# Optimization experiments

Hardware: AMD Instinct MI355X
Metric: run time of the kernel (lower is better)

Reference implementation:

```python
import jax, jax.numpy as jnp
import numpy as np

S = 4096            # num tokens (single causal sequence)
HID = 1024          # hidden_size
NH = 16             # num query heads
NKV = 4             # num kv heads
HD = 64             # head_dim
THETA = 10000.0
Q_SIZE = NH * HD
KV_SIZE = NKV * HD


def setup_inputs() -> dict:
    key = jax.random.key(0)
    k1, k2, k3 = jax.random.split(key, 3)
    return {
        "positions": jnp.arange(S, dtype=jnp.int32),
        "hidden_states": jax.random.normal(k1, (S, 2 * HID), dtype=jnp.float32),
        "w_qkv": jax.random.normal(k2, (Q_SIZE + 2 * KV_SIZE, 2 * HID), dtype=jnp.float32) * 0.02,
        "w_o": jax.random.normal(k3, (HID, Q_SIZE), dtype=jnp.float32) * 0.02,
    }


def _rope(x, positions):
    # x: [S, H, HD]; neox-style rotate-half RoPE
    half = HD // 2
    inv_freq = 1.0 / (THETA ** (jnp.arange(0, half, dtype=jnp.float32) / half))
    freqs = positions.astype(jnp.float32)[:, None] * inv_freq  # [S, half]
    cos = jnp.cos(freqs)[:, None, :]  # [S, 1, half]
    sin = jnp.sin(freqs)[:, None, :]
    x1, x2 = x[..., :half], x[..., half:]
    return jnp.concatenate([x1 * cos - x2 * sin, x2 * cos + x1 * sin], axis=-1)


def reference(positions, hidden_states, w_qkv, w_o):
    qkv = hidden_states @ w_qkv.T  # [S, Q_SIZE + 2*KV_SIZE]
    q = qkv[:, :Q_SIZE].reshape(S, NH, HD)
    k = qkv[:, Q_SIZE:Q_SIZE + KV_SIZE].reshape(S, NKV, HD)
    v = qkv[:, Q_SIZE + KV_SIZE:].reshape(S, NKV, HD)
    q = _rope(q, positions)
    k = _rope(k, positions)
    # GQA: group query heads over kv heads
    g = NH // NKV
    qg = q.reshape(S, NKV, g, HD)
    scale = HD ** -0.5
    scores = jnp.einsum("qhgd,thd->hgqt", qg, k) * scale  # [NKV, g, S, S]
    causal = positions[:, None] >= positions[None, :]      # [S, S]
    scores = jnp.where(causal[None, None], scores, jnp.finfo(scores.dtype).min)
    probs = jax.nn.softmax(scores, axis=-1)
    o = jnp.einsum("hgqt,thd->qhgd", probs, v).reshape(S, Q_SIZE)
    return o @ w_o.T  # [S, HID]
```

## Files before the change

### kernel.cpp

```cpp
#include <hip/hip_runtime.h>
#include <math.h>

#define S_LEN   4096
#define NHEADS  16
#define NKVH    4
#define HDIM    64
#define QKV_N   1536
#define HID2    2048
#define OUT_N   1024
#define QSCALE  0.18033688011112042f

typedef __attribute__((ext_vector_type(8))) __bf16 bf16x8;
typedef __attribute__((ext_vector_type(4))) __bf16 bf16x4;
typedef __attribute__((ext_vector_type(4))) float  f32x4;
typedef __attribute__((ext_vector_type(16))) float f32x16;
typedef __attribute__((ext_vector_type(4))) unsigned int u32x4;

#define GL_LDS16(gaddr, laddr)                                                  \
  __builtin_amdgcn_global_load_lds(                                             \
      (const __attribute__((address_space(1))) unsigned int*)(gaddr),           \
      (__attribute__((address_space(3))) unsigned int*)(laddr), 16, 0, 0)

__device__ __forceinline__ unsigned cvt_pk_bf16(float lo, float hi) {
  unsigned r;
  asm("v_cvt_pk_bf16_f32 %0, %1, %2" : "=v"(r) : "v"(lo), "v"(hi));
  return r;
}

__global__ __launch_bounds__(256) void cvt_all(const float* __restrict__ hid,
                                               const float* __restrict__ wq,
                                               const float* __restrict__ wo,
                                               __bf16* __restrict__ hid_bf,
                                               __bf16* __restrict__ wq_bf,
                                               __bf16* __restrict__ wo_bf) {
  const int n1 = S_LEN * HID2;
  const int n2 = QKV_N * HID2;
  int i = (blockIdx.x * blockDim.x + threadIdx.x) * 8;
  const float* src; __bf16* dst; int off;
  if (i < n1)           { src = hid; dst = hid_bf; off = i; }
  else if (i < n1 + n2) { src = wq;  dst = wq_bf;  off = i - n1; }
  else                  { src = wo;  dst = wo_bf;  off = i - n1 - n2; }
  float4 a = *(const float4*)(src + off);
  float4 b = *(const float4*)(src + off + 4);
  bf16x8 o = {(__bf16)a.x,(__bf16)a.y,(__bf16)a.z,(__bf16)a.w,
              (__bf16)b.x,(__bf16)b.y,(__bf16)b.z,(__bf16)b.w};
  *(bf16x8*)(dst + off) = o;
}

__global__ __launch_bounds__(256) void rope_table(const int* __restrict__ positions,
                                                  float* __restrict__ ct,
                                                  float* __restrict__ st) {
  int i = blockIdx.x * blockDim.x + threadIdx.x;
  int s = i >> 5, d = i & 31;
  double inv = pow(10000.0, -(double)d / 32.0);
  double fr = (double)positions[s] * inv;
  ct[i] = (float)cos(fr);
  st[i] = (float)sin(fr);
}

template<int BM, int EPI>
__global__ __launch_bounds__(256, (BM > 64 ? 2 : 3))
void gemm_db(const __bf16* __restrict__ A,
             const __bf16* __restrict__ B,
             void* __restrict__ Cp,
             const float* __restrict__ ct,
             const float* __restrict__ st,
             __bf16* __restrict__ qd,
             __bf16* __restrict__ kd,
             int M, int N, int K) {
  constexpr int TM  = BM / 32;
  constexpr int ASZ = BM * 32;
  constexpr int BSZ = 128 * 32;
  __shared__ __align__(16) __bf16 As[2 * 2 * ASZ];
  __shared__ __align__(16) __bf16 Bs[2 * 2 * BSZ];
  const int tid  = threadIdx.x;
  const int bm   = blockIdx.x, bn = blockIdx.y;
  const int wave = tid >> 6, lane = tid & 63;
  const int quad = lane >> 4, col = lane & 15;
  const int wm = (wave >> 1) * (BM / 2), wn = (wave & 1) * 64;

  const int lrow = lane >> 2, lcol = (lane & 3) * 8;
  const __bf16* Ag = A + (size_t)(bm * BM + wave * (BM / 4) + lrow) * K + lcol;
  const __bf16* Bg = B + (size_t)(bn * 128 + wave * 32 + lrow) * K + lcol;
  __bf16* AsW = As + wave * (BM / 4) * 32;
  __bf16* BsW = Bs + wave * 32 * 32;

  f32x4 acc[TM][4];
#pragma unroll
  for (int i = 0; i < TM; ++i)
#pragma unroll
    for (int j = 0; j < 4; ++j) acc[i][j] = (f32x4){0.f, 0.f, 0.f, 0.f};

  auto stage = [&](int buf, int kk) {
#pragma unroll
    for (int p = 0; p < 2; ++p) {
      const int koff = kk + p * 32;
      __bf16* ad = AsW + (buf * 2 + p) * ASZ;
      __bf16* bd = BsW + (buf * 2 + p) * BSZ;
#pragma unroll
      for (int u = 0; u < BM / 64; ++u)
        GL_LDS16(Ag + koff + (size_t)(u * 16) * K, ad + u * 16 * 32);
      GL_LDS16(Bg + koff,                  bd);
      GL_LDS16(Bg + koff + (size_t)16 * K, bd + 16 * 32);
    }
  };

  stage(0, 0);
  __syncthreads();

  int cur = 0;
  for (int kk = 0; kk < K; kk += 64) {
    if (kk + 64 < K) stage(cur ^ 1, kk + 64);

#pragma unroll
    for (int p = 0; p < 2; ++p) {
      const int pb = cur * 2 + p;
      bf16x8 a[TM], b[4];
#pragma unroll
      for (int tm = 0; tm < TM; ++tm)
        a[tm] = *(const bf16x8*)&As[pb * ASZ + (wm + tm * 16 + col) * 32 + quad * 8];
#pragma unroll
      for (int tn = 0; tn < 4; ++tn)
        b[tn] = *(const bf16x8*)&Bs[pb * BSZ + (wn + tn * 16 + col) * 32 + quad * 8];
#pragma unroll
      for (int tm = 0; tm < TM; ++tm)
#pragma unroll
        for (int tn = 0; tn < 4; ++tn)
          acc[tm][tn] = __builtin_amdgcn_mfma_f32_16x16x32_bf16(a[tm], b[tn], acc[tm][tn], 0, 0, 0);
    }

    __syncthreads();
    cur ^= 1;
  }

  if constexpr (EPI == 2) {
    if (bn < 10) {
      const float scl = (bn < 8) ? QSCALE : 1.0f;
      __bf16* dst    = (bn < 8) ? qd : kd;
      const int strd = (bn < 8) ? 1024 : 256;
      const int base = (bn < 8) ? 0 : 1024;
#pragma unroll
      for (int tm = 0; tm < TM; ++tm)
#pragma unroll
        for (int tn = 0; tn < 2; ++tn) {
          const int row0 = bm * BM + wm + tm * 16 + quad * 4;
          const int cg   = bn * 128 + wn + tn * 16 + col;
          const int dcol = cg - base;
          const int d    = tn * 16 + col;
#pragma unroll
          for (int r = 0; r < 4; ++r) {
            const int srow = row0 + r;
            float c  = ct[srow * 32 + d];
            float sn = st[srow * 32 + d];
            float x1 = acc[tm][tn][r], x2 = acc[tm][tn + 2][r];
            dst[(size_t)srow * strd + dcol]      = (__bf16)((x1 * c - x2 * sn) * scl);
            dst[(size_t)srow * strd + dcol + 32] = (__bf16)((x2 * c + x1 * sn) * scl);
          }
        }
    } else {
#pragma unroll
      for (int tm = 0; tm < TM; ++tm)
#pragma unroll
        for (int tn = 0; tn < 4; ++tn) {
          int row = bm * BM + wm + tm * 16 + quad * 4;
          int cg  = bn * 128 + wn + tn * 16 + col;
#pragma unroll
          for (int r = 0; r < 4; ++r)
            ((__bf16*)Cp)[(size_t)(row + r) * N + cg] = (__bf16)acc[tm][tn][r];
        }
    }
  } else {
#pragma unroll
    for (int tm = 0; tm < TM; ++tm)
#pragma unroll
      for (int tn = 0; tn < 4; ++tn) {
        int row = bm * BM + wm + tm * 16 + quad * 4;
        int cg  = bn * 128 + wn + tn * 16 + col;
#pragma unroll
        for (int r = 0; r < 4; ++r)
          ((float*)Cp)[(size_t)(row + r) * N + cg] = acc[tm][tn][r];
      }
  }
}

__global__ __launch_bounds__(256) void v_transpose(const __bf16* __restrict__ qkv,
                                                   __bf16* __restrict__ vT) {
  __shared__ __align__(16) __bf16 Ts[64][72];
  const int sb = blockIdx.x, kvh = blockIdx.y, t = threadIdx.x;
  const int r = t >> 2, c16 = (t & 3) * 16;
  const __bf16* src = qkv + (size_t)(sb * 64 + r) * QKV_N + 1280 + kvh * 64 + c16;
  bf16x8 v0 = *(const bf16x8*)src;
  bf16x8 v1 = *(const bf16x8*)(src + 8);
#pragma unroll
  for (int u = 0; u < 8; ++u) {
    Ts[c16 + u][r]     = v0[u];
    Ts[c16 + 8 + u][r] = v1[u];
  }
  __syncthreads();
  __bf16* dst = vT + ((size_t)kvh * 64 + r) * S_LEN + sb * 64 + c16;
  *(bf16x8*)dst       = *(const bf16x8*)&Ts[r][c16];
  *(bf16x8*)(dst + 8) = *(const bf16x8*)&Ts[r][c16 + 8];
}

__global__ __launch_bounds__(256, 4) void attn_split(const __bf16* __restrict__ qg,
                                                     const __bf16* __restrict__ kg,
                                                     const __bf16* __restrict__ vg,
                                                     __bf16* __restrict__ op0,
                                                     __bf16* __restrict__ op1,
                                                     float* __restrict__ lp) {
  __shared__ __align__(16) __bf16 lds[18432];
  __bf16* Ks = lds;
  __bf16* Vs = lds + 9216;

  const int tid = threadIdx.x;
  const int h = blockIdx.x;
  const int yy = blockIdx.y;
  const int qq = yy >> 1, split = yy & 1;
  const int qb = (qq < 16) ? qq : 47 - qq;
  const int kvh = h >> 2;
  const int wave = tid >> 6, lane = tid & 63;
  const int r31 = lane & 31, hi = lane >> 5;
  const int hi4 = hi * 4, hi8 = hi * 8;
  const int qbase = qb * 128 + wave * 32;
  const int kt0 = split * (qb + 1);
  const int ktEnd = kt0 + qb + 1;

  {
    const int r = tid >> 1, c = (tid & 1) * 32;
    const __bf16* src = qg + (size_t)(qb * 128 + r) * 1024 + h * 64 + c;
    __bf16* dq = lds + r * 72 + c;
    *(bf16x8*)(dq)      = *(const bf16x8*)(src);
    *(bf16x8*)(dq + 8)  = *(const bf16x8*)(src + 8);
    *(bf16x8*)(dq + 16) = *(const bf16x8*)(src + 16);
    *(bf16x8*)(dq + 24) = *(const bf16x8*)(src + 24);
  }

  const int sr = tid >> 2, sc = (tid & 3) * 16;
  const __bf16* kptr = kg + (size_t)sr * 256 + kvh * 64 + sc;
  const __bf16* vptr = vg + ((size_t)kvh * 64 + sr) * S_LEN + sc;
  bf16x8 kr0 = *(const bf16x8*)(kptr + (size_t)kt0 * 64 * 256);
  bf16x8 kr1 = *(const bf16x8*)(kptr + (size_t)kt0 * 64 * 256 + 8);
  bf16x8 vr0 = *(const bf16x8*)(vptr + (size_t)kt0 * 64);
  bf16x8 vr1 = *(const bf16x8*)(vptr + (size_t)kt0 * 64 + 8);

  __syncthreads();

  bf16x8 qf[4];
#pragma unroll
  for (int dc = 0; dc < 4; ++dc)
    qf[dc] = *(const bf16x8*)&lds[(wave * 32 + r31) * 72 + dc * 16 + hi8];

  __syncthreads();

  f32x16 fz;
#pragma unroll
  for (int g = 0; g < 16; ++g) fz[g] = 0.f;

  f32x16 o[2];
  o[0] = fz; o[1] = fz;
  float lacc = 0.f;

  for (int kt = kt0; kt < ktEnd; ++kt) {
    const int cur = (kt - kt0) & 1;
    {
      __bf16* kd = Ks + cur * 4608 + sr * 72 + sc;
      *(bf16x8*)kd       = kr0;
      *(bf16x8*)(kd + 8) = kr1;
      __bf16* vd = Vs + cur * 4608 + sr * 72 + sc;
      *(bf16x8*)vd       = vr0;
      *(bf16x8*)(vd + 8) = vr1;
    }
    if (kt + 1 < ktEnd) {
      const __bf16* kn = kptr + (size_t)(kt + 1) * 64 * 256;
      const __bf16* vn = vptr + (size_t)(kt + 1) * 64;
      kr0 = *(const bf16x8*)(kn);
      kr1 = *(const bf16x8*)(kn + 8);
      vr0 = *(const bf16x8*)(vn);
      vr1 = *(const bf16x8*)(vn + 8);
    }
    __syncthreads();

    if (kt * 64 > qbase + 31) continue;

    const bool full = (kt * 64 + 63 <= qbase);
    const int thr = qbase + r31 - kt * 64;

    bf16x8 pa[4];
#pragma unroll
    for (int kb = 0; kb < 2; ++kb) {
      bf16x8 kf0 = *(const bf16x8*)&Ks[cur * 4608 + (kb * 32 + r31) * 72 + hi8];
      f32x16 sf = __builtin_amdgcn_mfma_f32_32x32x16_bf16(kf0, qf[0], fz, 0, 0, 0);
#pragma unroll
      for (int dc = 1; dc < 4; ++dc) {
        bf16x8 kf = *(const bf16x8*)&Ks[cur * 4608 + (kb * 32 + r31) * 72 + dc * 16 + hi8];
        sf = __builtin_amdgcn_mfma_f32_32x32x16_bf16(kf, qf[dc], sf, 0, 0, 0);
      }
      float p[16];
#pragma unroll
      for (int g = 0; g < 16; ++g) {
        float e = __builtin_amdgcn_exp2f(sf[g]);
        if (!full) {
          const int krow = kb * 32 + (g & 3) + 8 * (g >> 2) + hi4;
          if (krow > thr) e = 0.f;
        }
        p[g] = e;
      }
#pragma unroll
      for (int m = 0; m < 4; ++m)
        lacc += (p[4 * m] + p[4 * m + 1]) + (p[4 * m + 2] + p[4 * m + 3]);
#pragma unroll
      for (int half = 0; half < 2; ++half) {
        unsigned a0 = cvt_pk_bf16(p[8 * half + 0], p[8 * half + 1]);
        unsigned a1 = cvt_pk_bf16(p[8 * half + 2], p[8 * half + 3]);
        unsigned b0 = cvt_pk_bf16(p[8 * half + 4], p[8 * half + 5]);
        unsigned b1 = cvt_pk_bf16(p[8 * half + 6], p[8 * half + 7]);
        asm("v_permlane32_swap_b32 %0, %1" : "+v"(a0), "+v"(b0));
        asm("v_permlane32_swap_b32 %0, %1" : "+v"(a1), "+v"(b1));
        u32x4 t = {a0, a1, b0, b1};
        pa[kb * 2 + half] = __builtin_bit_cast(bf16x8, t);
      }
    }

#pragma unroll
    for (int dt = 0; dt < 2; ++dt)
#pragma unroll
      for (int kc = 0; kc < 4; ++kc) {
        bf16x8 vf = *(const bf16x8*)&Vs[cur * 4608 + (dt * 32 + r31) * 72 + kc * 16 + hi8];
        o[dt] = __builtin_amdgcn_mfma_f32_32x32x16_bf16(pa[kc], vf, o[dt], 0, 0, 0);
      }
  }

  lacc += __shfl_xor(lacc, 32, 64);
  __syncthreads();
  float* lshw = (float*)lds + wave * 32;
  if (lane < 32) lshw[lane] = lacc;
  asm volatile("s_waitcnt lgkmcnt(0)" ::: "memory");

  __bf16* op = split ? op1 : op0;
#pragma unroll
  for (int g = 0; g < 16; ++g) {
    const int rl = (g & 3) + 8 * (g >> 2) + hi4;
    float l = lshw[rl];
    float linv = (l > 0.f) ? 1.f / l : 0.f;
    const size_t row = (size_t)(qb * 128 + wave * 32 + rl);
    op[row * 1024 + h * 64 + r31]      = (__bf16)(o[0][g] * linv);
    op[row * 1024 + h * 64 + 32 + r31] = (__bf16)(o[1][g] * linv);
  }
  if (lane < 32)
    lp[(size_t)(split * S_LEN + qb * 128 + wave * 32 + lane) * NHEADS + h] = lacc;
}

__global__ __launch_bounds__(256) void attn_combine(const __bf16* __restrict__ op0,
                                                    const __bf16* __restrict__ op1,
                                                    const float* __restrict__ lp,
                                                    __bf16* __restrict__ ob) {
  int i = blockIdx.x * 256 + threadIdx.x;
  int row = i >> 7, c8 = (i & 127) * 8;
  int h = c8 >> 6;
  float l0 = lp[(size_t)row * NHEADS + h];
  float l1 = lp[(size_t)(S_LEN + row) * NHEADS + h];
  float inv = 1.f / (l0 + l1);
  float w0 = l0 * inv, w1 = l1 * inv;
  bf16x8 a = *(const bf16x8*)(op0 + (size_t)row * 1024 + c8);
  bf16x8 b = *(const bf16x8*)(op1 + (size_t)row * 1024 + c8);
  bf16x8 o;
#pragma unroll
  for (int u = 0; u < 8; ++u)
    o[u] = (__bf16)((float)a[u] * w0 + (float)b[u] * w1);
  *(bf16x8*)(ob + (size_t)row * 1024 + c8) = o;
}

extern "C" void kernel_launch(void* const* d_in, const int* in_sizes, int n_in,
                              void* d_out, int out_size, void* d_ws, size_t ws_size,
                              hipStream_t stream) {
  const int*   positions = (const int*)d_in[0];
  const float* hidden    = (const float*)d_in[1];
  const float* w_qkv     = (const float*)d_in[2];
  const float* w_o       = (const float*)d_in[3];
  float* out = (float*)d_out;

  char* ws = (char*)d_ws;
  __bf16* qkv_bf  = (__bf16*)ws;
  __bf16* Opart0  = (__bf16*)ws;
  __bf16* attn_bf = (__bf16*)ws;
  float*  lpart   = (float*)(ws + 8388608);
  __bf16* hid_bf  = (__bf16*)(ws + 12582912);
  __bf16* vT      = (__bf16*)(ws + 23068672);
  float*  ct      = (float*)(ws + 29360128);
  float*  st      = (float*)(ws + 29884416);
  __bf16* wq_bf   = (__bf16*)(ws + 30408704);
  __bf16* Opart1  = (__bf16*)(ws + 30408704);
  __bf16* wo_bf   = (__bf16*)(ws + 38797312);
  __bf16* q_bf    = (__bf16*)d_out;
  __bf16* k_bf    = (__bf16*)((char*)d_out + 8388608);

  cvt_all<<<(S_LEN * HID2 + QKV_N * HID2 + OUT_N * OUT_N) / 8 / 256, 256, 0, stream>>>(
      hidden, w_qkv, w_o, hid_bf, wq_bf, wo_bf);
  rope_table<<<S_LEN * 32 / 256, 256, 0, stream>>>(positions, ct, st);

  gemm_db<128, 2><<<dim3(S_LEN / 128, QKV_N / 128), 256, 0, stream>>>(
      hid_bf, wq_bf, qkv_bf, ct, st, q_bf, k_bf, S_LEN, QKV_N, HID2);

  v_transpose<<<dim3(S_LEN / 64, NKVH), 256, 0, stream>>>(qkv_bf, vT);

  attn_split<<<dim3(NHEADS, 64), 256, 0, stream>>>(q_bf, k_bf, vT,
                                                   Opart0, Opart1, lpart);
  attn_combine<<<S_LEN * 128 / 256, 256, 0, stream>>>(Opart0, Opart1, lpart, attn_bf);

  gemm_db<64, 0><<<dim3(S_LEN / 64, OUT_N / 128), 256, 0, stream>>>(
      attn_bf, wo_bf, out, nullptr, nullptr, nullptr, nullptr, S_LEN, OUT_N, OUT_N);
}
```

Measured before the change: 215.9 us.

## Split attention KV range into variable chunk counts and swizzle LDS layout

```diff
diff --git a/kernel.cpp b/kernel.cpp
--- a/kernel.cpp
+++ b/kernel.cpp
@@ -202,42 +202,55 @@
   *(bf16x8*)(dst + 8) = *(const bf16x8*)&Ts[r][c16 + 8];
 }
 
-__global__ __launch_bounds__(256, 4) void attn_split(const __bf16* __restrict__ qg,
+__global__ __launch_bounds__(256, 5) void attn_split(const __bf16* __restrict__ qg,
                                                      const __bf16* __restrict__ kg,
                                                      const __bf16* __restrict__ vg,
                                                      __bf16* __restrict__ op0,
                                                      __bf16* __restrict__ op1,
+                                                     __bf16* __restrict__ op2,
+                                                     __bf16* __restrict__ op3,
                                                      float* __restrict__ lp) {
-  __shared__ __align__(16) __bf16 lds[18432];
+  __shared__ __align__(16) __bf16 lds[16384];
   __bf16* Ks = lds;
-  __bf16* Vs = lds + 9216;
+  __bf16* Vs = lds + 8192;
 
   const int tid = threadIdx.x;
   const int h = blockIdx.x;
-  const int yy = blockIdx.y;
-  const int qq = yy >> 1, split = yy & 1;
-  const int qb = (qq < 16) ? qq : 47 - qq;
+  const int y = blockIdx.y;
+  int qb, c;
+  if (y < 8)       { qb = y;                    c = 0; }
+  else if (y < 24) { qb = 8  + ((y - 8) >> 1);  c = (y - 8) & 1; }
+  else if (y < 48) { qb = 16 + (y - 24) / 3;    c = (y - 24) % 3; }
+  else             { qb = 24 + ((y - 48) >> 2); c = (y - 48) & 3; }
+  const int n   = 2 * (qb + 1);
+  const int nch = (qb >> 3) + 1;
+  const int bsz = n / nch, rm = n - bsz * nch;
+  const int kt0 = c * bsz + (c < rm ? c : rm);
+  const int ktEnd = kt0 + bsz + (c < rm ? 1 : 0);
+
   const int kvh = h >> 2;
   const int wave = tid >> 6, lane = tid & 63;
   const int r31 = lane & 31, hi = lane >> 5;
   const int hi4 = hi * 4, hi8 = hi * 8;
+  const int lsw = (r31 & 7) << 3;
   const int qbase = qb * 128 + wave * 32;
-  const int kt0 = split * (qb + 1);
-  const int ktEnd = kt0 + qb + 1;
 
   {
-    const int r = tid >> 1, c = (tid & 1) * 32;
-    const __bf16* src = qg + (size_t)(qb * 128 + r) * 1024 + h * 64 + c;
-    __bf16* dq = lds + r * 72 + c;
-    *(bf16x8*)(dq)      = *(const bf16x8*)(src);
-    *(bf16x8*)(dq + 8)  = *(const bf16x8*)(src + 8);
-    *(bf16x8*)(dq + 16) = *(const bf16x8*)(src + 16);
-    *(bf16x8*)(dq + 24) = *(const bf16x8*)(src + 24);
-  }
-
-  const int sr = tid >> 2, sc = (tid & 3) * 16;
-  const __bf16* kptr = kg + (size_t)sr * 256 + kvh * 64 + sc;
-  const __bf16* vptr = vg + ((size_t)kvh * 64 + sr) * S_LEN + sc;
+    const int r = tid >> 1, cc = (tid & 1) * 32;
+    const int rx = (r & 7) << 3;
+    const __bf16* src = qg + (size_t)(qb * 128 + r) * 1024 + h * 64 + cc;
+    __bf16* dq = lds + ((r * 64) & 8191);
+    dq = lds + r * 64;
+    *(bf16x8*)(dq + (( cc       ) ^ rx)) = *(const bf16x8*)(src);
+    *(bf16x8*)(dq + ((cc + 8 ) ^ rx))    = *(const bf16x8*)(src + 8);
+    *(bf16x8*)(dq + ((cc + 16) ^ rx))    = *(const bf16x8*)(src + 16);
+    *(bf16x8*)(dq + ((cc + 24) ^ rx))    = *(const bf16x8*)(src + 24);
+  }
+
+  const int sr = tid >> 2, se = (tid & 3) * 16;
+  const int ssw = (sr & 7) << 3;
+  const __bf16* kptr = kg + (size_t)sr * 256 + kvh * 64 + se;
+  const __bf16* vptr = vg + ((size_t)kvh * 64 + sr) * S_LEN + se;
   bf16x8 kr0 = *(const bf16x8*)(kptr + (size_t)kt0 * 64 * 256);
   bf16x8 kr1 = *(const bf16x8*)(kptr + (size_t)kt0 * 64 * 256 + 8);
   bf16x8 vr0 = *(const bf16x8*)(vptr + (size_t)kt0 * 64);
@@ -248,7 +261,7 @@
   bf16x8 qf[4];
 #pragma unroll
   for (int dc = 0; dc < 4; ++dc)
-    qf[dc] = *(const bf16x8*)&lds[(wave * 32 + r31) * 72 + dc * 16 + hi8];
+    qf[dc] = *(const bf16x8*)&lds[(wave * 32 + r31) * 64 + ((dc * 16 + hi8) ^ lsw)];
 
   __syncthreads();
 
@@ -263,12 +276,12 @@
   for (int kt = kt0; kt < ktEnd; ++kt) {
     const int cur = (kt - kt0) & 1;
     {
-      __bf16* kd = Ks + cur * 4608 + sr * 72 + sc;
-      *(bf16x8*)kd       = kr0;
-      *(bf16x8*)(kd + 8) = kr1;
-      __bf16* vd = Vs + cur * 4608 + sr * 72 + sc;
-      *(bf16x8*)vd       = vr0;
-      *(bf16x8*)(vd + 8) = vr1;
+      __bf16* kd = Ks + cur * 4096 + sr * 64;
+      *(bf16x8*)(kd + ( se      ^ ssw)) = kr0;
+      *(bf16x8*)(kd + ((se + 8) ^ ssw)) = kr1;
+      __bf16* vd = Vs + cur * 4096 + sr * 64;
+      *(bf16x8*)(vd + ( se      ^ ssw)) = vr0;
+      *(bf16x8*)(vd + ((se + 8) ^ ssw)) = vr1;
     }
     if (kt + 1 < ktEnd) {
       const __bf16* kn = kptr + (size_t)(kt + 1) * 64 * 256;
@@ -280,54 +293,54 @@
     }
     __syncthreads();
 
-    if (kt * 64 > qbase + 31) continue;
-
-    const bool full = (kt * 64 + 63 <= qbase);
-    const int thr = qbase + r31 - kt * 64;
-
-    bf16x8 pa[4];
-#pragma unroll
-    for (int kb = 0; kb < 2; ++kb) {
-      bf16x8 kf0 = *(const bf16x8*)&Ks[cur * 4608 + (kb * 32 + r31) * 72 + hi8];
-      f32x16 sf = __builtin_amdgcn_mfma_f32_32x32x16_bf16(kf0, qf[0], fz, 0, 0, 0);
-#pragma unroll
-      for (int dc = 1; dc < 4; ++dc) {
-        bf16x8 kf = *(const bf16x8*)&Ks[cur * 4608 + (kb * 32 + r31) * 72 + dc * 16 + hi8];
-        sf = __builtin_amdgcn_mfma_f32_32x32x16_bf16(kf, qf[dc], sf, 0, 0, 0);
+    if (kt * 64 <= qbase + 31) {
+      const bool full = (kt * 64 + 63 <= qbase);
+      const int thr = qbase + r31 - kt * 64;
+
+      bf16x8 pa[4];
+#pragma unroll
+      for (int kb = 0; kb < 2; ++kb) {
+        bf16x8 kf0 = *(const bf16x8*)&Ks[cur * 4096 + (kb * 32 + r31) * 64 + (hi8 ^ lsw)];
+        f32x16 sf = __builtin_amdgcn_mfma_f32_32x32x16_bf16(kf0, qf[0], fz, 0, 0, 0);
+#pragma unroll
+        for (int dc = 1; dc < 4; ++dc) {
+          bf16x8 kf = *(const bf16x8*)&Ks[cur * 4096 + (kb * 32 + r31) * 64 + ((dc * 16 + hi8) ^ lsw)];
+          sf = __builtin_amdgcn_mfma_f32_32x32x16_bf16(kf, qf[dc], sf, 0, 0, 0);
+        }
+        float p[16];
+#pragma unroll
+        for (int g = 0; g < 16; ++g) {
+          float e = __builtin_amdgcn_exp2f(sf[g]);
+          if (!full) {
+            const int krow = kb * 32 + (g & 3) + 8 * (g >> 2) + hi4;
+            if (krow > thr) e = 0.f;
+          }
+          p[g] = e;
+        }
+#pragma unroll
+        for (int mm = 0; mm < 4; ++mm)
+          lacc += (p[4 * mm] + p[4 * mm + 1]) + (p[4 * mm + 2] + p[4 * mm + 3]);
+#pragma unroll
+        for (int half = 0; half < 2; ++half) {
+          unsigned a0 = cvt_pk_bf16(p[8 * half + 0], p[8 * half + 1]);
+          unsigned a1 = cvt_pk_bf16(p[8 * half + 2], p[8 * half + 3]);
+          unsigned b0 = cvt_pk_bf16(p[8 * half + 4], p[8 * half + 5]);
+          unsigned b1 = cvt_pk_bf16(p[8 * half + 6], p[8 * half + 7]);
+          asm("v_permlane32_swap_b32 %0, %1" : "+v"(a0), "+v"(b0));
+          asm("v_permlane32_swap_b32 %0, %1" : "+v"(a1), "+v"(b1));
+          u32x4 t = {a0, a1, b0, b1};
+          pa[kb * 2 + half] = __builtin_bit_cast(bf16x8, t);
+        }
       }
-      float p[16];
-#pragma unroll
-      for (int g = 0; g < 16; ++g) {
-        float e = __builtin_amdgcn_exp2f(sf[g]);
-        if (!full) {
-          const int krow = kb * 32 + (g & 3) + 8 * (g >> 2) + hi4;
-          if (krow > thr) e = 0.f;
-        }
-        p[g] = e;
-      }
-#pragma unroll
-      for (int m = 0; m < 4; ++m)
-        lacc += (p[4 * m] + p[4 * m + 1]) + (p[4 * m + 2] + p[4 * m + 3]);
-#pragma unroll
-      for (int half = 0; half < 2; ++half) {
-        unsigned a0 = cvt_pk_bf16(p[8 * half + 0], p[8 * half + 1]);
-        unsigned a1 = cvt_pk_bf16(p[8 * half + 2], p[8 * half + 3]);
-        unsigned b0 = cvt_pk_bf16(p[8 * half + 4], p[8 * half + 5]);
-        unsigned b1 = cvt_pk_bf16(p[8 * half + 6], p[8 * half + 7]);
-        asm("v_permlane32_swap_b32 %0, %1" : "+v"(a0), "+v"(b0));
-        asm("v_permlane32_swap_b32 %0, %1" : "+v"(a1), "+v"(b1));
-        u32x4 t = {a0, a1, b0, b1};
-        pa[kb * 2 + half] = __builtin_bit_cast(bf16x8, t);
-      }
-    }
-
-#pragma unroll
-    for (int dt = 0; dt < 2; ++dt)
-#pragma unroll
-      for (int kc = 0; kc < 4; ++kc) {
-        bf16x8 vf = *(const bf16x8*)&Vs[cur * 4608 + (dt * 32 + r31) * 72 + kc * 16 + hi8];
-        o[dt] = __builtin_amdgcn_mfma_f32_32x32x16_bf16(pa[kc], vf, o[dt], 0, 0, 0);
-      }
+
+#pragma unroll
+      for (int dt = 0; dt < 2; ++dt)
+#pragma unroll
+        for (int kc = 0; kc < 4; ++kc) {
+          bf16x8 vf = *(const bf16x8*)&Vs[cur * 4096 + (dt * 32 + r31) * 64 + ((kc * 16 + hi8) ^ lsw)];
+          o[dt] = __builtin_amdgcn_mfma_f32_32x32x16_bf16(pa[kc], vf, o[dt], 0, 0, 0);
+        }
+    }
   }
 
   lacc += __shfl_xor(lacc, 32, 64);
@@ -336,7 +349,7 @@
   if (lane < 32) lshw[lane] = lacc;
   asm volatile("s_waitcnt lgkmcnt(0)" ::: "memory");
 
-  __bf16* op = split ? op1 : op0;
+  __bf16* op = (c == 0) ? op0 : (c == 1) ? op1 : (c == 2) ? op2 : op3;
 #pragma unroll
   for (int g = 0; g < 16; ++g) {
     const int rl = (g & 3) + 8 * (g >> 2) + hi4;
@@ -347,26 +360,46 @@
     op[row * 1024 + h * 64 + 32 + r31] = (__bf16)(o[1][g] * linv);
   }
   if (lane < 32)
-    lp[(size_t)(split * S_LEN + qb * 128 + wave * 32 + lane) * NHEADS + h] = lacc;
+    lp[(size_t)(c * S_LEN + qb * 128 + wave * 32 + lane) * NHEADS + h] = lacc;
 }
 
 __global__ __launch_bounds__(256) void attn_combine(const __bf16* __restrict__ op0,
                                                     const __bf16* __restrict__ op1,
+                                                    const __bf16* __restrict__ op2,
+                                                    const __bf16* __restrict__ op3,
                                                     const float* __restrict__ lp,
                                                     __bf16* __restrict__ ob) {
   int i = blockIdx.x * 256 + threadIdx.x;
   int row = i >> 7, c8 = (i & 127) * 8;
   int h = c8 >> 6;
+  const int nch = (row >> 10) + 1;
   float l0 = lp[(size_t)row * NHEADS + h];
-  float l1 = lp[(size_t)(S_LEN + row) * NHEADS + h];
-  float inv = 1.f / (l0 + l1);
-  float w0 = l0 * inv, w1 = l1 * inv;
+  float l1 = (nch > 1) ? lp[(size_t)(S_LEN + row) * NHEADS + h] : 0.f;
+  float l2 = (nch > 2) ? lp[(size_t)(2 * S_LEN + row) * NHEADS + h] : 0.f;
+  float l3 = (nch > 3) ? lp[(size_t)(3 * S_LEN + row) * NHEADS + h] : 0.f;
+  float inv = 1.f / (l0 + l1 + l2 + l3);
+  float acc[8];
   bf16x8 a = *(const bf16x8*)(op0 + (size_t)row * 1024 + c8);
-  bf16x8 b = *(const bf16x8*)(op1 + (size_t)row * 1024 + c8);
+#pragma unroll
+  for (int u = 0; u < 8; ++u) acc[u] = (float)a[u] * l0;
+  if (nch > 1) {
+    bf16x8 b = *(const bf16x8*)(op1 + (size_t)row * 1024 + c8);
+#pragma unroll
+    for (int u = 0; u < 8; ++u) acc[u] += (float)b[u] * l1;
+  }
+  if (nch > 2) {
+    bf16x8 b = *(const bf16x8*)(op2 + (size_t)row * 1024 + c8);
+#pragma unroll
+    for (int u = 0; u < 8; ++u) acc[u] += (float)b[u] * l2;
+  }
+  if (nch > 3) {
+    bf16x8 b = *(const bf16x8*)(op3 + (size_t)row * 1024 + c8);
+#pragma unroll
+    for (int u = 0; u < 8; ++u) acc[u] += (float)b[u] * l3;
+  }
   bf16x8 o;
 #pragma unroll
-  for (int u = 0; u < 8; ++u)
-    o[u] = (__bf16)((float)a[u] * w0 + (float)b[u] * w1);
+  for (int u = 0; u < 8; ++u) o[u] = (__bf16)(acc[u] * inv);
   *(bf16x8*)(ob + (size_t)row * 1024 + c8) = o;
 }
 
@@ -393,19 +426,23 @@
   __bf16* wo_bf   = (__bf16*)(ws + 38797312);
   __bf16* q_bf    = (__bf16*)d_out;
   __bf16* k_bf    = (__bf16*)((char*)d_out + 8388608);
+  __bf16* Opart3  = (__bf16*)((char*)d_out + 10485760 - (size_t)3072 * 2048);
+  __bf16* Opart2  = (__bf16*)((char*)d_out + 12582912 - (size_t)2048 * 2048);
 
   cvt_all<<<(S_LEN * HID2 + QKV_N * HID2 + OUT_N * OUT_N) / 8 / 256, 256, 0, stream>>>(
       hidden, w_qkv, w_o, hid_bf, wq_bf, wo_bf);
   rope_table<<<S_LEN * 32 / 256, 256, 0, stream>>>(positions, ct, st);
 
-  gemm_db<128, 2><<<dim3(S_LEN / 128, QKV_N / 128), 256, 0, stream>>>(
+  gemm_db<64, 2><<<dim3(S_LEN / 64, QKV_N / 128), 256, 0, stream>>>(
       hid_bf, wq_bf, qkv_bf, ct, st, q_bf, k_bf, S_LEN, QKV_N, HID2);
 
   v_transpose<<<dim3(S_LEN / 64, NKVH), 256, 0, stream>>>(qkv_bf, vT);
 
-  attn_split<<<dim3(NHEADS, 64), 256, 0, stream>>>(q_bf, k_bf, vT,
-                                                   Opart0, Opart1, lpart);
-  attn_combine<<<S_LEN * 128 / 256, 256, 0, stream>>>(Opart0, Opart1, lpart, attn_bf);
+  attn_split<<<dim3(NHEADS, 80), 256, 0, stream>>>(q_bf, k_bf, vT,
+                                                   Opart0, Opart1, Opart2, Opart3,
+                                                   lpart);
+  attn_combine<<<S_LEN * 128 / 256, 256, 0, stream>>>(Opart0, Opart1, Opart2, Opart3,
+                                                      lpart, attn_bf);
 
   gemm_db<64, 0><<<dim3(S_LEN / 64, OUT_N / 128), 256, 0, stream>>>(
       attn_bf, wo_bf, out, nullptr, nullptr, nullptr, nullptr, S_LEN, OUT_N, OUT_N);
```

Result: slower. 338.2 us (+56.7%).
